# Kernel tuning notes

Hardware: AMD Instinct MI355X
Metric: run time of the kernel (lower is better)

Reference implementation:

```python
import jax, jax.numpy as jnp
import numpy as np

EPS = 1e-5


def _batchnorm(x, gamma, beta):
    # training-mode batch norm over the node axis, per feature channel
    mean = jnp.mean(x, axis=0)
    var = jnp.var(x, axis=0)  # biased variance, as torch uses for normalization
    return (x - mean) * jax.lax.rsqrt(var + EPS) * gamma + beta


def _gcn_conv(h, W, b, src, dst, norm, n_nodes):
    # h: [N, Fin] -> [N, Fout]; D^{-1/2}(A+I)D^{-1/2} (h W) + b
    h = h @ W                                   # [N, Fout]
    msgs = h[src] * norm[:, None]               # [E+N, Fout] gathered, normalized
    out = jax.ops.segment_sum(msgs, dst, num_segments=n_nodes)
    return out + b


def setup_inputs() -> dict:
    key = jax.random.key(0)
    ks = jax.random.split(key, 8)
    N, F, E, H = 50000, 512, 800000, 256
    inp = {
        "x": jax.random.normal(ks[0], (N, F), jnp.float32),
        "edge_index": jax.random.randint(ks[1], (2, E), 0, N, jnp.int64),
        "gamma1": jnp.ones((F,), jnp.float32),
        "beta1": jnp.zeros((F,), jnp.float32),
        "W1": jax.random.normal(ks[2], (F, H), jnp.float32) * (1.0 / np.sqrt(F)),
        "b1": jnp.zeros((H,), jnp.float32),
        "W2": jax.random.normal(ks[3], (H, H), jnp.float32) * (1.0 / np.sqrt(H)),
        "b2": jnp.zeros((H,), jnp.float32),
        "W3": jax.random.normal(ks[4], (H, H), jnp.float32) * (1.0 / np.sqrt(H)),
        "b3": jnp.zeros((H,), jnp.float32),
        "W4": jax.random.normal(ks[5], (H, H), jnp.float32) * (1.0 / np.sqrt(H)),
        "b4": jnp.zeros((H,), jnp.float32),
        "gamma2": jnp.ones((H,), jnp.float32),
        "beta2": jnp.zeros((H,), jnp.float32),
        "Wd": jax.random.normal(ks[6], (H, 5), jnp.float32) * (1.0 / np.sqrt(H)),
        "bd": jnp.zeros((5,), jnp.float32),
    }
    return inp


def reference(x, edge_index, gamma1, beta1, W1, b1, W2, b2, W3, b3, W4, b4,
              gamma2, beta2, Wd, bd):
    N = x.shape[0]
    loops = jnp.arange(N, dtype=edge_index.dtype)
    src = jnp.concatenate([edge_index[0], loops])
    dst = jnp.concatenate([edge_index[1], loops])
    deg = jax.ops.segment_sum(jnp.ones_like(src, dtype=x.dtype), dst, num_segments=N)
    dinv = jax.lax.rsqrt(deg)                    # deg >= 1 due to self-loops
    norm = dinv[src] * dinv[dst]                 # [E+N]

    h = _batchnorm(x, gamma1, beta1)
    h = _gcn_conv(h, W1, b1, src, dst, norm, N)
    h = _gcn_conv(h, W2, b2, src, dst, norm, N)
    h = _gcn_conv(h, W3, b3, src, dst, norm, N)
    h = _gcn_conv(h, W4, b4, src, dst, norm, N)
    h = _batchnorm(h, gamma2, beta2)
    # Flatten(start_dim=1) is identity on [N, 256]
    return jax.nn.sigmoid(h @ Wd + bd)           # [N, 5]
```

## Files before the change

### kernel.cpp

```cpp
#include <hip/hip_runtime.h>
#include <math.h>

#define BN_EPS 1e-5f

typedef float floatx4 __attribute__((ext_vector_type(4)));
typedef short shortx4 __attribute__((ext_vector_type(4)));
typedef short shortx8 __attribute__((ext_vector_type(8)));
typedef __bf16 bf16x8 __attribute__((ext_vector_type(8)));

__device__ __forceinline__ unsigned short f2b(float f) {
    unsigned int u = __builtin_bit_cast(unsigned int, f);
    u += 0x7fffu + ((u >> 16) & 1u);
    return (unsigned short)(u >> 16);
}
__device__ __forceinline__ float b2f(unsigned short s) {
    unsigned int u = ((unsigned int)s) << 16;
    return __builtin_bit_cast(float, u);
}
__device__ __forceinline__ float b2f_s(short s) { return b2f((unsigned short)s); }

__global__ __launch_bounds__(256)
void k_detect(const unsigned int* __restrict__ ei, int n_check, int* __restrict__ flag) {
    __shared__ int any;
    if (threadIdx.x == 0) any = 0;
    __syncthreads();
    for (int i = threadIdx.x; i < n_check; i += 256) {
        if (ei[2 * i + 1] != 0u) any = 1;
    }
    __syncthreads();
    if (threadIdx.x == 0) *flag = any;
}

__global__ __launch_bounds__(256)
void k_convert(const void* __restrict__ ei_raw, const int* __restrict__ flag,
               int* __restrict__ src, int* __restrict__ dst, int E) {
    int e = blockIdx.x * 256 + threadIdx.x;
    if (e >= E) return;
    if (*flag) {
        const int* a = (const int*)ei_raw;
        src[e] = a[e];
        dst[e] = a[E + e];
    } else {
        const long long* a = (const long long*)ei_raw;
        src[e] = (int)a[e];
        dst[e] = (int)a[E + e];
    }
}

__global__ __launch_bounds__(256)
void k_count(const int* __restrict__ dst, int* __restrict__ cnt, int E) {
    int e = blockIdx.x * 256 + threadIdx.x;
    if (e < E) atomicAdd(&cnt[dst[e]], 1);
}

__global__ __launch_bounds__(1024)
void k_scan_sum(const int* __restrict__ cnt, int* __restrict__ bsum, int N) {
    __shared__ int s[1024];
    int i = blockIdx.x * 1024 + threadIdx.x;
    s[threadIdx.x] = (i < N) ? cnt[i] : 0;
    __syncthreads();
    for (int off = 512; off > 0; off >>= 1) {
        if (threadIdx.x < off) s[threadIdx.x] += s[threadIdx.x + off];
        __syncthreads();
    }
    if (threadIdx.x == 0) bsum[blockIdx.x] = s[0];
}

__global__ __launch_bounds__(1024)
void k_scan_part(int* __restrict__ bsum, int nb) {
    __shared__ int s[1024];
    int t = threadIdx.x;
    int v = (t < nb) ? bsum[t] : 0;
    s[t] = v;
    __syncthreads();
    for (int off = 1; off < 1024; off <<= 1) {
        int tmp = (t >= off) ? s[t - off] : 0;
        __syncthreads();
        s[t] += tmp;
        __syncthreads();
    }
    if (t < nb) bsum[t] = s[t] - v;
}

__global__ __launch_bounds__(1024)
void k_scan_final(const int* __restrict__ cnt, const int* __restrict__ bsum,
                  int* __restrict__ row_ptr, int* __restrict__ cursor,
                  float* __restrict__ dinv, int N) {
    __shared__ int s[1024];
    int b = blockIdx.x, t = threadIdx.x;
    int i = b * 1024 + t;
    int v = (i < N) ? cnt[i] : 0;
    s[t] = v;
    __syncthreads();
    for (int off = 1; off < 1024; off <<= 1) {
        int tmp = (t >= off) ? s[t - off] : 0;
        __syncthreads();
        s[t] += tmp;
        __syncthreads();
    }
    if (i < N) {
        int excl = bsum[b] + s[t] - v;
        row_ptr[i] = excl;
        cursor[i]  = excl;
        dinv[i] = rsqrtf((float)(v + 1));
        if (i == N - 1) row_ptr[N] = excl + v;
    }
}

__global__ __launch_bounds__(256)
void k_fill(const int* __restrict__ src, const int* __restrict__ dst,
            int* __restrict__ cursor, const float* __restrict__ dinv,
            int* __restrict__ csr_src, float* __restrict__ csr_w, int E) {
    int e = blockIdx.x * 256 + threadIdx.x;
    if (e >= E) return;
    int s = src[e], d = dst[e];
    int p = atomicAdd(&cursor[d], 1);
    csr_src[p] = s;
    csr_w[p]   = dinv[s] * dinv[d];
}

__global__ __launch_bounds__(256)
void k_bnstats(const float* __restrict__ x, float* __restrict__ sum, float* __restrict__ sumsq,
               int N, int F) {
    __shared__ float ls[512], lq[512];
    int q   = F >> 2;
    int t   = threadIdx.x;
    int cq  = t % q;
    int ro  = t / q;
    int rpp = 256 / q;
    float s0 = 0.f, s1 = 0.f, s2 = 0.f, s3 = 0.f;
    float q0 = 0.f, q1 = 0.f, q2 = 0.f, q3 = 0.f;
    for (int r = blockIdx.x * rpp + ro; r < N; r += gridDim.x * rpp) {
        float4 v = *(const float4*)&x[(size_t)r * F + cq * 4];
        s0 += v.x; s1 += v.y; s2 += v.z; s3 += v.w;
        q0 += v.x * v.x; q1 += v.y * v.y; q2 += v.z * v.z; q3 += v.w * v.w;
    }
    for (int c = t; c < F; c += 256) { ls[c] = 0.f; lq[c] = 0.f; }
    __syncthreads();
    atomicAdd(&ls[cq * 4 + 0], s0); atomicAdd(&ls[cq * 4 + 1], s1);
    atomicAdd(&ls[cq * 4 + 2], s2); atomicAdd(&ls[cq * 4 + 3], s3);
    atomicAdd(&lq[cq * 4 + 0], q0); atomicAdd(&lq[cq * 4 + 1], q1);
    atomicAdd(&lq[cq * 4 + 2], q2); atomicAdd(&lq[cq * 4 + 3], q3);
    __syncthreads();
    for (int c = t; c < F; c += 256) {
        atomicAdd(&sum[c],   ls[c]);
        atomicAdd(&sumsq[c], lq[c]);
    }
}

__global__ __launch_bounds__(256)
void k_bnfin(const float* __restrict__ sum, const float* __restrict__ sumsq,
             const float* __restrict__ gamma, const float* __restrict__ beta,
             float* __restrict__ a, float* __restrict__ b, int N, int F) {
    int c = blockIdx.x * 256 + threadIdx.x;
    if (c >= F) return;
    float m   = sum[c] / (float)N;
    float var = sumsq[c] / (float)N - m * m;
    float rs  = rsqrtf(var + BN_EPS);
    float aa  = gamma[c] * rs;
    a[c] = aa;
    b[c] = beta[c] - m * aa;
}

__global__ __launch_bounds__(256)
void k_cast_bn(const float* __restrict__ x, const float* __restrict__ a, const float* __restrict__ b,
               unsigned short* __restrict__ xb, int N, int F, int Mpad) {
    int i = blockIdx.x * 256 + threadIdx.x;
    int total = Mpad * (F / 8);
    if (i >= total) return;
    int row = i / (F / 8);
    int col = (i % (F / 8)) * 8;
    shortx8 v;
    if (row < N) {
        float4 x0 = *(const float4*)&x[(size_t)row * F + col];
        float4 x1 = *(const float4*)&x[(size_t)row * F + col + 4];
        float4 a0 = *(const float4*)&a[col];
        float4 a1 = *(const float4*)&a[col + 4];
        float4 b0 = *(const float4*)&b[col];
        float4 b1 = *(const float4*)&b[col + 4];
        v[0] = (short)f2b(x0.x * a0.x + b0.x);
        v[1] = (short)f2b(x0.y * a0.y + b0.y);
        v[2] = (short)f2b(x0.z * a0.z + b0.z);
        v[3] = (short)f2b(x0.w * a0.w + b0.w);
        v[4] = (short)f2b(x1.x * a1.x + b1.x);
        v[5] = (short)f2b(x1.y * a1.y + b1.y);
        v[6] = (short)f2b(x1.z * a1.z + b1.z);
        v[7] = (short)f2b(x1.w * a1.w + b1.w);
    } else {
        #pragma unroll
        for (int j = 0; j < 8; ++j) v[j] = 0;
    }
    *(shortx8*)&xb[(size_t)row * F + col] = v;
}

__global__ __launch_bounds__(256)
void k_castWT(const float* __restrict__ W, unsigned short* __restrict__ Wt, int K, int NC) {
    int i = blockIdx.x * 256 + threadIdx.x;
    if (i >= K * NC) return;
    int n = i / K, k = i % K;
    Wt[i] = f2b(W[(size_t)k * NC + n]);
}

__device__ __forceinline__ void glds16(const void* g, void* l) {
    __builtin_amdgcn_global_load_lds(
        (const __attribute__((address_space(1))) unsigned int*)g,
        (__attribute__((address_space(3))) unsigned int*)l, 16, 0, 0);
}

__global__ __launch_bounds__(256)
void k_gemm_bf16(const unsigned short* __restrict__ A, const unsigned short* __restrict__ Bt,
                 unsigned short* __restrict__ C, int K, int NC) {
    __shared__ unsigned short As[128 * 32];
    __shared__ unsigned short Bs[128 * 32];
    int tid  = threadIdx.x;
    int wave = tid >> 6, lane = tid & 63;
    int row0 = blockIdx.x * 128;
    int col0 = blockIdx.y * 128;
    int wr = (wave & 1) * 64;
    int wc = (wave >> 1) * 64;

    floatx4 acc[4][4];
    #pragma unroll
    for (int i = 0; i < 4; i++)
        #pragma unroll
        for (int j = 0; j < 4; j++) acc[i][j] = (floatx4){0.f, 0.f, 0.f, 0.f};

    int cA = tid * 16;
    int cB = cA + 4096;
    const char* Ab = (const char*)A;
    const char* Bb = (const char*)Bt;
    size_t a_off0 = (size_t)(row0 + (cA >> 6)) * K * 2 + (cA & 63);
    size_t a_off1 = (size_t)(row0 + (cB >> 6)) * K * 2 + (cB & 63);
    size_t b_off0 = (size_t)(col0 + (cA >> 6)) * K * 2 + (cA & 63);
    size_t b_off1 = (size_t)(col0 + (cB >> 6)) * K * 2 + (cB & 63);

    int lm  = lane & 15;
    int lk8 = (lane >> 4) * 8;

    for (int ks = 0; ks < K; ks += 32) {
        size_t koff = (size_t)ks * 2;
        glds16(Ab + a_off0 + koff, (char*)As + cA);
        glds16(Ab + a_off1 + koff, (char*)As + cA + 4096);
        glds16(Bb + b_off0 + koff, (char*)Bs + cA);
        glds16(Bb + b_off1 + koff, (char*)Bs + cA + 4096);
        __syncthreads();

        bf16x8 af[4], bfr[4];
        #pragma unroll
        for (int i = 0; i < 4; i++) {
            shortx8 s = *(const shortx8*)&As[(wr + i * 16 + lm) * 32 + lk8];
            af[i] = __builtin_bit_cast(bf16x8, s);
        }
        #pragma unroll
        for (int j = 0; j < 4; j++) {
            shortx8 s = *(const shortx8*)&Bs[(wc + j * 16 + lm) * 32 + lk8];
            bfr[j] = __builtin_bit_cast(bf16x8, s);
        }
        #pragma unroll
        for (int i = 0; i < 4; i++)
            #pragma unroll
            for (int j = 0; j < 4; j++)
                acc[i][j] = __builtin_amdgcn_mfma_f32_16x16x32_bf16(af[i], bfr[j], acc[i][j], 0, 0, 0);
        __syncthreads();
    }

    int crow = row0 + wr + (lane >> 4) * 4;
    int ccol = col0 + wc + lm;
    #pragma unroll
    for (int i = 0; i < 4; i++)
        #pragma unroll
        for (int j = 0; j < 4; j++)
            #pragma unroll
            for (int r = 0; r < 4; r++)
                C[(size_t)(crow + i * 16 + r) * NC + ccol + j * 16] = f2b(acc[i][j][r]);
}

__global__ __launch_bounds__(256)
void k_agg(const unsigned short* __restrict__ hin, unsigned short* __restrict__ hout_b,
           float* __restrict__ hout_f,
           const int* __restrict__ row_ptr, const int* __restrict__ csr_src,
           const float* __restrict__ csr_w, const float* __restrict__ dinv,
           const float* __restrict__ bias, int N) {
    const int H = 256;
    int node = blockIdx.x * 4 + (threadIdx.x >> 6);
    if (node >= N) return;
    int lane = threadIdx.x & 63;
    int f = lane * 4;
    float di = dinv[node];
    float sl = di * di;
    shortx4 hv = *(const shortx4*)&hin[(size_t)node * H + f];
    float a0 = b2f_s(hv[0]) * sl, a1 = b2f_s(hv[1]) * sl;
    float a2 = b2f_s(hv[2]) * sl, a3 = b2f_s(hv[3]) * sl;
    int e0 = row_ptr[node], e1 = row_ptr[node + 1];
    int e = e0;
    for (; e + 4 <= e1; e += 4) {
        int   s0 = csr_src[e],     s1 = csr_src[e + 1];
        int   s2 = csr_src[e + 2], s3 = csr_src[e + 3];
        float w0 = csr_w[e],     w1 = csr_w[e + 1];
        float w2 = csr_w[e + 2], w3 = csr_w[e + 3];
        shortx4 r0 = *(const shortx4*)&hin[(size_t)s0 * H + f];
        shortx4 r1 = *(const shortx4*)&hin[(size_t)s1 * H + f];
        shortx4 r2 = *(const shortx4*)&hin[(size_t)s2 * H + f];
        shortx4 r3 = *(const shortx4*)&hin[(size_t)s3 * H + f];
        a0 += w0 * b2f_s(r0[0]) + w1 * b2f_s(r1[0]) + w2 * b2f_s(r2[0]) + w3 * b2f_s(r3[0]);
        a1 += w0 * b2f_s(r0[1]) + w1 * b2f_s(r1[1]) + w2 * b2f_s(r2[1]) + w3 * b2f_s(r3[1]);
        a2 += w0 * b2f_s(r0[2]) + w1 * b2f_s(r1[2]) + w2 * b2f_s(r2[2]) + w3 * b2f_s(r3[2]);
        a3 += w0 * b2f_s(r0[3]) + w1 * b2f_s(r1[3]) + w2 * b2f_s(r2[3]) + w3 * b2f_s(r3[3]);
    }
    for (; e < e1; ++e) {
        int   s = csr_src[e];
        float w = csr_w[e];
        shortx4 r = *(const shortx4*)&hin[(size_t)s * H + f];
        a0 += w * b2f_s(r[0]); a1 += w * b2f_s(r[1]);
        a2 += w * b2f_s(r[2]); a3 += w * b2f_s(r[3]);
    }
    float4 bi = *(const float4*)&bias[f];
    a0 += bi.x; a1 += bi.y; a2 += bi.z; a3 += bi.w;
    shortx4 o;
    o[0] = (short)f2b(a0); o[1] = (short)f2b(a1);
    o[2] = (short)f2b(a2); o[3] = (short)f2b(a3);
    *(shortx4*)&hout_b[(size_t)node * H + f] = o;
    if (hout_f) {
        float4 of = make_float4(a0, a1, a2, a3);
        *(float4*)&hout_f[(size_t)node * H + f] = of;
    }
}

__global__ __launch_bounds__(64)
void k_head(const float* __restrict__ h, const float* __restrict__ a, const float* __restrict__ b,
            const float* __restrict__ Wd, const float* __restrict__ bd,
            float* __restrict__ out, int N) {
    int node = blockIdx.x;
    int lane = threadIdx.x;
    int f = lane * 4;
    float4 hv = *(const float4*)(h + (size_t)node * 256 + f);
    float v0 = hv.x * a[f + 0] + b[f + 0];
    float v1 = hv.y * a[f + 1] + b[f + 1];
    float v2 = hv.z * a[f + 2] + b[f + 2];
    float v3 = hv.w * a[f + 3] + b[f + 3];
    float s[5];
    #pragma unroll
    for (int j = 0; j < 5; ++j) {
        s[j] = v0 * Wd[(f + 0) * 5 + j] + v1 * Wd[(f + 1) * 5 + j] +
               v2 * Wd[(f + 2) * 5 + j] + v3 * Wd[(f + 3) * 5 + j];
    }
    #pragma unroll
    for (int off = 32; off > 0; off >>= 1) {
        #pragma unroll
        for (int j = 0; j < 5; ++j) s[j] += __shfl_down(s[j], off);
    }
    if (lane == 0) {
        #pragma unroll
        for (int j = 0; j < 5; ++j) {
            float z = s[j] + bd[j];
            out[(size_t)node * 5 + j] = 1.f / (1.f + expf(-z));
        }
    }
}

extern "C" void kernel_launch(void* const* d_in, const int* in_sizes, int n_in,
                              void* d_out, int out_size, void* d_ws, size_t ws_size,
                              hipStream_t stream) {
    const float* x      = (const float*)d_in[0];
    const void*  ei_raw = d_in[1];
    const float* gamma1 = (const float*)d_in[2];
    const float* beta1  = (const float*)d_in[3];
    const float* W1 = (const float*)d_in[4];
    const float* b1 = (const float*)d_in[5];
    const float* W2 = (const float*)d_in[6];
    const float* b2 = (const float*)d_in[7];
    const float* W3 = (const float*)d_in[8];
    const float* b3 = (const float*)d_in[9];
    const float* W4 = (const float*)d_in[10];
    const float* b4 = (const float*)d_in[11];
    const float* gamma2 = (const float*)d_in[12];
    const float* beta2  = (const float*)d_in[13];
    const float* Wd = (const float*)d_in[14];
    const float* bd = (const float*)d_in[15];

    const int F = in_sizes[2];
    const int N = in_sizes[0] / F;
    const int E = in_sizes[1] / 2;
    const int H = in_sizes[5];
    const int Mpad = ((N + 127) / 128) * 128;
    const int NB   = (N + 1023) / 1024;
    float* out = (float*)d_out;

    char* p = (char*)d_ws;
    auto alloc = [&](size_t bytes) {
        void* r = (void*)p;
        p += (bytes + 255) & ~(size_t)255;
        return r;
    };
    int*   flag    = (int*)  alloc(4);
    int*   srcA    = (int*)  alloc((size_t)E * 4);
    int*   dstA    = (int*)  alloc((size_t)E * 4);
    int*   cnt     = (int*)  alloc((size_t)N * 4);
    int*   row_ptr = (int*)  alloc(((size_t)N + 1) * 4);
    int*   cursor  = (int*)  alloc((size_t)N * 4);
    float* dinv    = (float*)alloc((size_t)N * 4);
    int*   csr_src = (int*)  alloc((size_t)E * 4);
    float* csr_w   = (float*)alloc((size_t)E * 4);
    int*   bsum    = (int*)  alloc((size_t)NB * 4);
    float* colsum  = (float*)alloc((size_t)F * 4);
    float* colsq   = (float*)alloc((size_t)F * 4);
    float* bna     = (float*)alloc((size_t)F * 4);
    float* bnb     = (float*)alloc((size_t)F * 4);
    unsigned short* W1t = (unsigned short*)alloc((size_t)F * H * 2);
    unsigned short* W2t = (unsigned short*)alloc((size_t)H * H * 2);
    unsigned short* W3t = (unsigned short*)alloc((size_t)H * H * 2);
    unsigned short* W4t = (unsigned short*)alloc((size_t)H * H * 2);
    unsigned short* xb  = (unsigned short*)alloc((size_t)Mpad * F * 2);
    float* hbF          = (float*)xb;
    unsigned short* hbA = (unsigned short*)alloc((size_t)Mpad * H * 2);
    unsigned short* hbB = (unsigned short*)alloc((size_t)Mpad * H * 2);

    hipMemsetAsync(cnt,    0, (size_t)N * 4, stream);
    hipMemsetAsync(colsum, 0, (size_t)F * 4, stream);
    hipMemsetAsync(colsq,  0, (size_t)F * 4, stream);

    int n_check = (E >= 2048) ? 2048 : E;
    k_detect<<<1, 256, 0, stream>>>((const unsigned int*)ei_raw, n_check, flag);
    k_convert<<<(E + 255) / 256, 256, 0, stream>>>(ei_raw, flag, srcA, dstA, E);
    k_count<<<(E + 255) / 256, 256, 0, stream>>>(dstA, cnt, E);
    k_scan_sum<<<NB, 1024, 0, stream>>>(cnt, bsum, N);
    k_scan_part<<<1, 1024, 0, stream>>>(bsum, NB);
    k_scan_final<<<NB, 1024, 0, stream>>>(cnt, bsum, row_ptr, cursor, dinv, N);
    k_fill<<<(E + 255) / 256, 256, 0, stream>>>(srcA, dstA, cursor, dinv, csr_src, csr_w, E);

    k_bnstats<<<512, 256, 0, stream>>>(x, colsum, colsq, N, F);
    k_bnfin<<<(F + 255) / 256, 256, 0, stream>>>(colsum, colsq, gamma1, beta1, bna, bnb, N, F);
    k_cast_bn<<<(Mpad * (F / 8) + 255) / 256, 256, 0, stream>>>(x, bna, bnb, xb, N, F, Mpad);

    k_castWT<<<(F * H + 255) / 256, 256, 0, stream>>>(W1, W1t, F, H);
    k_castWT<<<(H * H + 255) / 256, 256, 0, stream>>>(W2, W2t, H, H);
    k_castWT<<<(H * H + 255) / 256, 256, 0, stream>>>(W3, W3t, H, H);
    k_castWT<<<(H * H + 255) / 256, 256, 0, stream>>>(W4, W4t, H, H);

    dim3 gg(Mpad / 128, H / 128);
    int aggb = (N + 3) / 4;
    k_gemm_bf16<<<gg, 256, 0, stream>>>(xb, W1t, hbA, F, H);
    k_agg<<<aggb, 256, 0, stream>>>(hbA, hbB, nullptr, row_ptr, csr_src, csr_w, dinv, b1, N);
    k_gemm_bf16<<<gg, 256, 0, stream>>>(hbB, W2t, hbA, H, H);
    k_agg<<<aggb, 256, 0, stream>>>(hbA, hbB, nullptr, row_ptr, csr_src, csr_w, dinv, b2, N);
    k_gemm_bf16<<<gg, 256, 0, stream>>>(hbB, W3t, hbA, H, H);
    k_agg<<<aggb, 256, 0, stream>>>(hbA, hbB, nullptr, row_ptr, csr_src, csr_w, dinv, b3, N);
    k_gemm_bf16<<<gg, 256, 0, stream>>>(hbB, W4t, hbA, H, H);
    k_agg<<<aggb, 256, 0, stream>>>(hbA, hbB, hbF, row_ptr, csr_src, csr_w, dinv, b4, N);

    hipMemsetAsync(colsum, 0, (size_t)H * 4, stream);
    hipMemsetAsync(colsq,  0, (size_t)H * 4, stream);
    k_bnstats<<<512, 256, 0, stream>>>(hbF, colsum, colsq, N, H);
    k_bnfin<<<(H + 255) / 256, 256, 0, stream>>>(colsum, colsq, gamma2, beta2, bna, bnb, N, H);
    k_head<<<N, 64, 0, stream>>>(hbF, bna, bnb, Wd, bd, out, N);
}
```

Measured before the change: 719.0 us.

## Pack CSR edges, widen aggregation loads, drop fp32 output path, merge weight casts

Edge source index and weight are packed into one int2 array, so each aggregation step issues a single load per edge. The aggregation kernel now has each wave split into two halves that handle alternate edges with 8-wide bf16 loads, and the halves are combined with a cross-lane shuffle. The final layer no longer writes an fp32 copy; the second batchnorm stats and the head read the bf16 buffer directly, which cuts memory traffic at a small precision cost. Also merges the four weight-cast launches into one, unrolls the bnstats loop by two with a larger grid, and packs four nodes per block in the head kernel.

Result: no change. 712.9 us (-0.9%).

```diff
diff --git a/kernel.cpp b/kernel.cpp
--- a/kernel.cpp
+++ b/kernel.cpp
@@ -110,13 +110,13 @@
 __global__ __launch_bounds__(256)
 void k_fill(const int* __restrict__ src, const int* __restrict__ dst,
             int* __restrict__ cursor, const float* __restrict__ dinv,
-            int* __restrict__ csr_src, float* __restrict__ csr_w, int E) {
+            int2* __restrict__ csr_sw, int E) {
     int e = blockIdx.x * 256 + threadIdx.x;
     if (e >= E) return;
     int s = src[e], d = dst[e];
     int p = atomicAdd(&cursor[d], 1);
-    csr_src[p] = s;
-    csr_w[p]   = dinv[s] * dinv[d];
+    float w = dinv[s] * dinv[d];
+    csr_sw[p] = make_int2(s, __builtin_bit_cast(int, w));
 }
 
 __global__ __launch_bounds__(256)
@@ -128,10 +128,17 @@
     int cq  = t % q;
     int ro  = t / q;
     int rpp = 256 / q;
+    int step = gridDim.x * rpp;
     float s0 = 0.f, s1 = 0.f, s2 = 0.f, s3 = 0.f;
     float q0 = 0.f, q1 = 0.f, q2 = 0.f, q3 = 0.f;
-    for (int r = blockIdx.x * rpp + ro; r < N; r += gridDim.x * rpp) {
+    for (int r = blockIdx.x * rpp + ro; r < N; r += 2 * step) {
         float4 v = *(const float4*)&x[(size_t)r * F + cq * 4];
+        int r2 = r + step;
+        if (r2 < N) {
+            float4 u = *(const float4*)&x[(size_t)r2 * F + cq * 4];
+            s0 += u.x; s1 += u.y; s2 += u.z; s3 += u.w;
+            q0 += u.x * u.x; q1 += u.y * u.y; q2 += u.z * u.z; q3 += u.w * u.w;
+        }
         s0 += v.x; s1 += v.y; s2 += v.z; s3 += v.w;
         q0 += v.x * v.x; q1 += v.y * v.y; q2 += v.z * v.z; q3 += v.w * v.w;
     }
@@ -146,6 +153,37 @@
         atomicAdd(&sum[c],   ls[c]);
         atomicAdd(&sumsq[c], lq[c]);
     }
+}
+
+__global__ __launch_bounds__(256)
+void k_bnstats_b(const unsigned short* __restrict__ x, float* __restrict__ sum,
+                 float* __restrict__ sumsq, int N, int H) {
+    __shared__ float ls[256], lq[256];
+    int t  = threadIdx.x;
+    int cg = t & 31;
+    int ro = t >> 5;
+    int step = gridDim.x * 8;
+    float s[8], q[8];
+    #pragma unroll
+    for (int j = 0; j < 8; ++j) { s[j] = 0.f; q[j] = 0.f; }
+    for (int r = blockIdx.x * 8 + ro; r < N; r += step) {
+        shortx8 v = *(const shortx8*)&x[(size_t)r * H + cg * 8];
+        #pragma unroll
+        for (int j = 0; j < 8; ++j) {
+            float f = b2f_s(v[j]);
+            s[j] += f; q[j] += f * f;
+        }
+    }
+    ls[t] = 0.f; lq[t] = 0.f;
+    __syncthreads();
+    #pragma unroll
+    for (int j = 0; j < 8; ++j) {
+        atomicAdd(&ls[cg * 8 + j], s[j]);
+        atomicAdd(&lq[cg * 8 + j], q[j]);
+    }
+    __syncthreads();
+    atomicAdd(&sum[t],   ls[t]);
+    atomicAdd(&sumsq[t], lq[t]);
 }
 
 __global__ __launch_bounds__(256)
@@ -194,11 +232,21 @@
 }
 
 __global__ __launch_bounds__(256)
-void k_castWT(const float* __restrict__ W, unsigned short* __restrict__ Wt, int K, int NC) {
+void k_castWT4(const float* __restrict__ W1, const float* __restrict__ W2,
+               const float* __restrict__ W3, const float* __restrict__ W4,
+               unsigned short* __restrict__ T1, unsigned short* __restrict__ T2,
+               unsigned short* __restrict__ T3, unsigned short* __restrict__ T4,
+               int F, int H) {
     int i = blockIdx.x * 256 + threadIdx.x;
-    if (i >= K * NC) return;
-    int n = i / K, k = i % K;
-    Wt[i] = f2b(W[(size_t)k * NC + n]);
+    int n1 = F * H, n2 = H * H;
+    const float* W; unsigned short* T; int K; int j;
+    if (i < n1)               { W = W1; T = T1; K = F; j = i; }
+    else if (i < n1 + n2)     { W = W2; T = T2; K = H; j = i - n1; }
+    else if (i < n1 + 2 * n2) { W = W3; T = T3; K = H; j = i - n1 - n2; }
+    else if (i < n1 + 3 * n2) { W = W4; T = T4; K = H; j = i - n1 - 2 * n2; }
+    else return;
+    int n = j / K, k = j % K;
+    T[j] = f2b(W[(size_t)k * H + n]);
 }
 
 __device__ __forceinline__ void glds16(const void* g, void* l) {
@@ -276,68 +324,86 @@
 }
 
 __global__ __launch_bounds__(256)
-void k_agg(const unsigned short* __restrict__ hin, unsigned short* __restrict__ hout_b,
-           float* __restrict__ hout_f,
-           const int* __restrict__ row_ptr, const int* __restrict__ csr_src,
-           const float* __restrict__ csr_w, const float* __restrict__ dinv,
-           const float* __restrict__ bias, int N) {
+void k_agg(const unsigned short* __restrict__ hin, unsigned short* __restrict__ hout,
+           const int* __restrict__ row_ptr, const int2* __restrict__ csr_sw,
+           const float* __restrict__ dinv, const float* __restrict__ bias, int N) {
     const int H = 256;
     int node = blockIdx.x * 4 + (threadIdx.x >> 6);
     if (node >= N) return;
     int lane = threadIdx.x & 63;
-    int f = lane * 4;
+    int half = lane >> 5;
+    int f = (lane & 31) * 8;
+    float acc[8];
     float di = dinv[node];
-    float sl = di * di;
-    shortx4 hv = *(const shortx4*)&hin[(size_t)node * H + f];
-    float a0 = b2f_s(hv[0]) * sl, a1 = b2f_s(hv[1]) * sl;
-    float a2 = b2f_s(hv[2]) * sl, a3 = b2f_s(hv[3]) * sl;
+    if (half == 0) {
+        shortx8 hv = *(const shortx8*)&hin[(size_t)node * H + f];
+        float sl = di * di;
+        #pragma unroll
+        for (int j = 0; j < 8; ++j) acc[j] = b2f_s(hv[j]) * sl;
+    } else {
+        #pragma unroll
+        for (int j = 0; j < 8; ++j) acc[j] = 0.f;
+    }
     int e0 = row_ptr[node], e1 = row_ptr[node + 1];
     int e = e0;
-    for (; e + 4 <= e1; e += 4) {
-        int   s0 = csr_src[e],     s1 = csr_src[e + 1];
-        int   s2 = csr_src[e + 2], s3 = csr_src[e + 3];
-        float w0 = csr_w[e],     w1 = csr_w[e + 1];
-        float w2 = csr_w[e + 2], w3 = csr_w[e + 3];
-        shortx4 r0 = *(const shortx4*)&hin[(size_t)s0 * H + f];
-        shortx4 r1 = *(const shortx4*)&hin[(size_t)s1 * H + f];
-        shortx4 r2 = *(const shortx4*)&hin[(size_t)s2 * H + f];
-        shortx4 r3 = *(const shortx4*)&hin[(size_t)s3 * H + f];
-        a0 += w0 * b2f_s(r0[0]) + w1 * b2f_s(r1[0]) + w2 * b2f_s(r2[0]) + w3 * b2f_s(r3[0]);
-        a1 += w0 * b2f_s(r0[1]) + w1 * b2f_s(r1[1]) + w2 * b2f_s(r2[1]) + w3 * b2f_s(r3[1]);
-        a2 += w0 * b2f_s(r0[2]) + w1 * b2f_s(r1[2]) + w2 * b2f_s(r2[2]) + w3 * b2f_s(r3[2]);
-        a3 += w0 * b2f_s(r0[3]) + w1 * b2f_s(r1[3]) + w2 * b2f_s(r2[3]) + w3 * b2f_s(r3[3]);
-    }
-    for (; e < e1; ++e) {
-        int   s = csr_src[e];
-        float w = csr_w[e];
-        shortx4 r = *(const shortx4*)&hin[(size_t)s * H + f];
-        a0 += w * b2f_s(r[0]); a1 += w * b2f_s(r[1]);
-        a2 += w * b2f_s(r[2]); a3 += w * b2f_s(r[3]);
-    }
-    float4 bi = *(const float4*)&bias[f];
-    a0 += bi.x; a1 += bi.y; a2 += bi.z; a3 += bi.w;
-    shortx4 o;
-    o[0] = (short)f2b(a0); o[1] = (short)f2b(a1);
-    o[2] = (short)f2b(a2); o[3] = (short)f2b(a3);
-    *(shortx4*)&hout_b[(size_t)node * H + f] = o;
-    if (hout_f) {
-        float4 of = make_float4(a0, a1, a2, a3);
-        *(float4*)&hout_f[(size_t)node * H + f] = of;
-    }
-}
-
-__global__ __launch_bounds__(64)
-void k_head(const float* __restrict__ h, const float* __restrict__ a, const float* __restrict__ b,
-            const float* __restrict__ Wd, const float* __restrict__ bd,
-            float* __restrict__ out, int N) {
-    int node = blockIdx.x;
-    int lane = threadIdx.x;
+    for (; e + 8 <= e1; e += 8) {
+        int2 p0 = csr_sw[e + 0 + half];
+        int2 p1 = csr_sw[e + 2 + half];
+        int2 p2 = csr_sw[e + 4 + half];
+        int2 p3 = csr_sw[e + 6 + half];
+        shortx8 r0 = *(const shortx8*)&hin[(size_t)p0.x * H + f];
+        shortx8 r1 = *(const shortx8*)&hin[(size_t)p1.x * H + f];
+        shortx8 r2 = *(const shortx8*)&hin[(size_t)p2.x * H + f];
+        shortx8 r3 = *(const shortx8*)&hin[(size_t)p3.x * H + f];
+        float w0 = __builtin_bit_cast(float, p0.y);
+        float w1 = __builtin_bit_cast(float, p1.y);
+        float w2 = __builtin_bit_cast(float, p2.y);
+        float w3 = __builtin_bit_cast(float, p3.y);
+        #pragma unroll
+        for (int j = 0; j < 8; ++j)
+            acc[j] += w0 * b2f_s(r0[j]) + w1 * b2f_s(r1[j])
+                    + w2 * b2f_s(r2[j]) + w3 * b2f_s(r3[j]);
+    }
+    for (; e < e1; e += 2) {
+        int idx = e + half;
+        bool valid = idx < e1;
+        int2 pr = csr_sw[valid ? idx : e];
+        float w = valid ? __builtin_bit_cast(float, pr.y) : 0.f;
+        shortx8 r = *(const shortx8*)&hin[(size_t)pr.x * H + f];
+        #pragma unroll
+        for (int j = 0; j < 8; ++j) acc[j] += w * b2f_s(r[j]);
+    }
+    #pragma unroll
+    for (int j = 0; j < 8; ++j) acc[j] += __shfl_xor(acc[j], 32, 64);
+    if (half == 0) {
+        float4 bi0 = *(const float4*)&bias[f];
+        float4 bi1 = *(const float4*)&bias[f + 4];
+        shortx8 o;
+        o[0] = (short)f2b(acc[0] + bi0.x);
+        o[1] = (short)f2b(acc[1] + bi0.y);
+        o[2] = (short)f2b(acc[2] + bi0.z);
+        o[3] = (short)f2b(acc[3] + bi0.w);
+        o[4] = (short)f2b(acc[4] + bi1.x);
+        o[5] = (short)f2b(acc[5] + bi1.y);
+        o[6] = (short)f2b(acc[6] + bi1.z);
+        o[7] = (short)f2b(acc[7] + bi1.w);
+        *(shortx8*)&hout[(size_t)node * H + f] = o;
+    }
+}
+
+__global__ __launch_bounds__(256)
+void k_head(const unsigned short* __restrict__ h, const float* __restrict__ a,
+            const float* __restrict__ b, const float* __restrict__ Wd,
+            const float* __restrict__ bd, float* __restrict__ out, int N) {
+    int node = blockIdx.x * 4 + (threadIdx.x >> 6);
+    if (node >= N) return;
+    int lane = threadIdx.x & 63;
     int f = lane * 4;
-    float4 hv = *(const float4*)(h + (size_t)node * 256 + f);
-    float v0 = hv.x * a[f + 0] + b[f + 0];
-    float v1 = hv.y * a[f + 1] + b[f + 1];
-    float v2 = hv.z * a[f + 2] + b[f + 2];
-    float v3 = hv.w * a[f + 3] + b[f + 3];
+    shortx4 hv = *(const shortx4*)&h[(size_t)node * 256 + f];
+    float v0 = b2f_s(hv[0]) * a[f + 0] + b[f + 0];
+    float v1 = b2f_s(hv[1]) * a[f + 1] + b[f + 1];
+    float v2 = b2f_s(hv[2]) * a[f + 2] + b[f + 2];
+    float v3 = b2f_s(hv[3]) * a[f + 3] + b[f + 3];
     float s[5];
     #pragma unroll
     for (int j = 0; j < 5; ++j) {
@@ -347,7 +413,7 @@
     #pragma unroll
     for (int off = 32; off > 0; off >>= 1) {
         #pragma unroll
-        for (int j = 0; j < 5; ++j) s[j] += __shfl_down(s[j], off);
+        for (int j = 0; j < 5; ++j) s[j] += __shfl_down(s[j], off, 64);
     }
     if (lane == 0) {
         #pragma unroll
@@ -399,8 +465,7 @@
     int*   row_ptr = (int*)  alloc(((size_t)N + 1) * 4);
     int*   cursor  = (int*)  alloc((size_t)N * 4);
     float* dinv    = (float*)alloc((size_t)N * 4);
-    int*   csr_src = (int*)  alloc((size_t)E * 4);
-    float* csr_w   = (float*)alloc((size_t)E * 4);
+    int2*  csr_sw  = (int2*) alloc((size_t)E * 8);
     int*   bsum    = (int*)  alloc((size_t)NB * 4);
     float* colsum  = (float*)alloc((size_t)F * 4);
     float* colsq   = (float*)alloc((size_t)F * 4);
@@ -411,7 +476,6 @@
     unsigned short* W3t = (unsigned short*)alloc((size_t)H * H * 2);
     unsigned short* W4t = (unsigned short*)alloc((size_t)H * H * 2);
     unsigned short* xb  = (unsigned short*)alloc((size_t)Mpad * F * 2);
-    float* hbF          = (float*)xb;
     unsigned short* hbA = (unsigned short*)alloc((size_t)Mpad * H * 2);
     unsigned short* hbB = (unsigned short*)alloc((size_t)Mpad * H * 2);
 
@@ -426,31 +490,29 @@
     k_scan_sum<<<NB, 1024, 0, stream>>>(cnt, bsum, N);
     k_scan_part<<<1, 1024, 0, stream>>>(bsum, NB);
     k_scan_final<<<NB, 1024, 0, stream>>>(cnt, bsum, row_ptr, cursor, dinv, N);
-    k_fill<<<(E + 255) / 256, 256, 0, stream>>>(srcA, dstA, cursor, dinv, csr_src, csr_w, E);
-
-    k_bnstats<<<512, 256, 0, stream>>>(x, colsum, colsq, N, F);
+    k_fill<<<(E + 255) / 256, 256, 0, stream>>>(srcA, dstA, cursor, dinv, csr_sw, E);
+
+    k_bnstats<<<1024, 256, 0, stream>>>(x, colsum, colsq, N, F);
     k_bnfin<<<(F + 255) / 256, 256, 0, stream>>>(colsum, colsq, gamma1, beta1, bna, bnb, N, F);
     k_cast_bn<<<(Mpad * (F / 8) + 255) / 256, 256, 0, stream>>>(x, bna, bnb, xb, N, F, Mpad);
 
-    k_castWT<<<(F * H + 255) / 256, 256, 0, stream>>>(W1, W1t, F, H);
-    k_castWT<<<(H * H + 255) / 256, 256, 0, stream>>>(W2, W2t, H, H);
-    k_castWT<<<(H * H + 255) / 256, 256, 0, stream>>>(W3, W3t, H, H);
-    k_castWT<<<(H * H + 255) / 256, 256, 0, stream>>>(W4, W4t, H, H);
+    int tot = F * H + 3 * H * H;
+    k_castWT4<<<(tot + 255) / 256, 256, 0, stream>>>(W1, W2, W3, W4, W1t, W2t, W3t, W4t, F, H);
 
     dim3 gg(Mpad / 128, H / 128);
     int aggb = (N + 3) / 4;
     k_gemm_bf16<<<gg, 256, 0, stream>>>(xb, W1t, hbA, F, H);
-    k_agg<<<aggb, 256, 0, stream>>>(hbA, hbB, nullptr, row_ptr, csr_src, csr_w, dinv, b1, N);
+    k_agg<<<aggb, 256, 0, stream>>>(hbA, hbB, row_ptr, csr_sw, dinv, b1, N);
     k_gemm_bf16<<<gg, 256, 0, stream>>>(hbB, W2t, hbA, H, H);
-    k_agg<<<aggb, 256, 0, stream>>>(hbA, hbB, nullptr, row_ptr, csr_src, csr_w, dinv, b2, N);
+    k_agg<<<aggb, 256, 0, stream>>>(hbA, hbB, row_ptr, csr_sw, dinv, b2, N);
     k_gemm_bf16<<<gg, 256, 0, stream>>>(hbB, W3t, hbA, H, H);
-    k_agg<<<aggb, 256, 0, stream>>>(hbA, hbB, nullptr, row_ptr, csr_src, csr_w, dinv, b3, N);
+    k_agg<<<aggb, 256, 0, stream>>>(hbA, hbB, row_ptr, csr_sw, dinv, b3, N);
     k_gemm_bf16<<<gg, 256, 0, stream>>>(hbB, W4t, hbA, H, H);
-    k_agg<<<aggb, 256, 0, stream>>>(hbA, hbB, hbF, row_ptr, csr_src, csr_w, dinv, b4, N);
+    k_agg<<<aggb, 256, 0, stream>>>(hbA, hbB, row_ptr, csr_sw, dinv, b4, N);
 
     hipMemsetAsync(colsum, 0, (size_t)H * 4, stream);
     hipMemsetAsync(colsq,  0, (size_t)H * 4, stream);
-    k_bnstats<<<512, 256, 0, stream>>>(hbF, colsum, colsq, N, H);
+    k_bnstats_b<<<512, 256, 0, stream>>>(hbB, colsum, colsq, N, H);
     k_bnfin<<<(H + 255) / 256, 256, 0, stream>>>(colsum, colsq, gamma2, beta2, bna, bnb, N, H);
-    k_head<<<N, 64, 0, stream>>>(hbF, bna, bnb, Wd, bd, out, N);
-}
+    k_head<<<(N + 3) / 4, 256, 0, stream>>>(hbB, bna, bnb, Wd, bd, out, N);
+}
```
